# Kernel tuning notes

Measured on AMD Instinct MI355X. Metric: run time of the kernel, lower is better.

Reference implementation:

```python
import jax, jax.numpy as jnp
import numpy as np

B, N, D = 16, 512, 12
HID, HEADS = 32, 4
C = HID // HEADS  # per-head channels = 8


def setup_inputs() -> dict:
    key = jax.random.key(0)
    ks = jax.random.split(key, 12)
    s = 0.1
    return {
        "x": jax.random.normal(ks[0], (B, N, D), dtype=jnp.float32),
        "adj": jax.random.randint(ks[1], (B, N, N), 0, 2, dtype=jnp.int32),
        # node_proj: Linear(D, HID)
        "Wp": jax.random.normal(ks[2], (HID, D), dtype=jnp.float32) * s,
        "bp": jax.random.normal(ks[3], (HID,), dtype=jnp.float32) * s,
        # GATConv lin: Linear(HID, HEADS*C, bias=False)
        "Wg": jax.random.normal(ks[4], (HEADS * C, HID), dtype=jnp.float32) * s,
        "att_src": jax.random.normal(ks[5], (HEADS, C), dtype=jnp.float32) * s,
        "att_dst": jax.random.normal(ks[6], (HEADS, C), dtype=jnp.float32) * s,
        "bias_g": jax.random.normal(ks[7], (HEADS * C,), dtype=jnp.float32) * s,
        # edge_mlp: Linear(2*HID, HID) -> ReLU -> Linear(HID, 1) -> Sigmoid
        "W1": jax.random.normal(ks[8], (HID, 2 * HID), dtype=jnp.float32) * s,
        "b1": jax.random.normal(ks[9], (HID,), dtype=jnp.float32) * s,
        "w2": jax.random.normal(ks[10], (HID,), dtype=jnp.float32) * s,
        "b2": jax.random.normal(ks[11], (1,), dtype=jnp.float32) * s,
    }


def reference(x, adj, Wp, bp, Wg, att_src, att_dst, bias_g, W1, b1, w2, b2):
    Bq, Nq, _ = x.shape
    adj_b = adj != 0
    eye = jnp.eye(Nq, dtype=bool)

    # node_proj + ReLU
    h = jax.nn.relu(jnp.einsum('bnd,hd->bnh', x, Wp) + bp)  # [B,N,HID]

    # GATConv (PyG semantics): messages flow src=i (row) -> dst=j (col),
    # self-loops removed then re-added => diagonal forced on.
    g = jnp.einsum('bnd,kd->bnk', h, Wg).reshape(Bq, Nq, HEADS, C)  # [B,N,H,C]
    a_s = jnp.einsum('bnhc,hc->bnh', g, att_src)  # [B,N,H]
    a_d = jnp.einsum('bnhc,hc->bnh', g, att_dst)  # [B,N,H]
    logits = jax.nn.leaky_relu(a_s[:, :, None, :] + a_d[:, None, :, :], 0.2)  # [B,i,j,H]
    mask_sl = adj_b | eye
    logits = jnp.where(mask_sl[..., None], logits, -1e9)
    alpha = jax.nn.softmax(logits, axis=1)  # softmax over source i per target j
    h_gnn = jnp.einsum('bijh,bihc->bjhc', alpha, g).reshape(Bq, Nq, HEADS * C) + bias_g

    # edge MLP on all (i,j) pairs: cat([h_i, h_j]) -> split W1
    W1i, W1j = W1[:, :HID], W1[:, HID:]
    ti = jnp.einsum('bnd,hd->bnh', h_gnn, W1i)  # [B,N,HID] (row / i part)
    tj = jnp.einsum('bnd,hd->bnh', h_gnn, W1j)  # [B,N,HID] (col / j part)
    hidden = jax.nn.relu(ti[:, :, None, :] + tj[:, None, :, :] + b1)  # [B,N,N,HID]
    score = jax.nn.sigmoid(jnp.einsum('bijh,h->bij', hidden, w2) + b2[0])

    out_mask = adj_b & ~eye
    return jnp.where(out_mask, score, jnp.float32(0.0))
```

## Files before the change

kernel.cpp:

```cpp
#include <hip/hip_runtime.h>
#include <cstdint>

#define Bq 16
#define Nq 512
#define Dq 12
#define HID 32
#define HEADS 4
#define Cq 8

#define OFF_G     0u
#define OFF_AS    262144u
#define OFF_AD    294912u
#define OFF_TIT   327680u
#define OFF_TJB   589824u
#define OFF_PACK  851968u

__global__ __launch_bounds__(256) void k0_node(
    const float* __restrict__ x, const float* __restrict__ Wp, const float* __restrict__ bp,
    const float* __restrict__ Wg, const float* __restrict__ att_src,
    const float* __restrict__ att_dst, float* __restrict__ ws) {
    __shared__ float xs[8 * Dq];
    __shared__ float hs[8][HID];
    int n_sub = threadIdx.x >> 5;
    int k = threadIdx.x & 31;
    int node0 = blockIdx.x * 8;
    if (threadIdx.x < 8 * Dq) xs[threadIdx.x] = x[(size_t)node0 * Dq + threadIdx.x];
    __syncthreads();
    float s = bp[k];
#pragma unroll
    for (int d = 0; d < Dq; d++) s = fmaf(Wp[k * Dq + d], xs[n_sub * Dq + d], s);
    hs[n_sub][k] = s > 0.f ? s : 0.f;
    __syncthreads();
    float g = 0.f;
#pragma unroll
    for (int d = 0; d < HID; d++) g = fmaf(Wg[k * HID + d], hs[n_sub][d], g);
    int nid = node0 + n_sub;
    ws[OFF_G + (size_t)nid * HID + k] = g;
    float ss = g * att_src[k];
    float sd = g * att_dst[k];
#pragma unroll
    for (int off = 1; off < 8; off <<= 1) {
        ss += __shfl_xor(ss, off);
        sd += __shfl_xor(sd, off);
    }
    if ((k & 7) == 0) {
        int h = k >> 3;
        ws[OFF_AS + (size_t)nid * HEADS + h] = ss;
        ws[OFF_AD + (size_t)nid * HEADS + h] = sd;
    }
}

__global__ __launch_bounds__(256, 2) void k1_fused(
    const int* __restrict__ adj, const float* __restrict__ bias_g,
    const float* __restrict__ W1, const float* __restrict__ b1,
    float* __restrict__ ws) {
    int b = blockIdx.y;
    int j0 = blockIdx.x * 16;
    int t = threadIdx.x;
    int jl = t & 15;
    int ig = t >> 4;
    int j = j0 + jl;

    __shared__ float gs[64 * 36];
    __shared__ float ass[64 * 4];
    __shared__ float red[36 * 16 * 5];
    __shared__ float hgs[16 * 36];
    __shared__ float W1s[32 * 68];

    {
        const float4* src = (const float4*)W1;
        for (int k = t; k < 512; k += 256) {
            int h = k >> 4, q = k & 15;
            *(float4*)&W1s[h * 68 + q * 4] = src[k];
        }
    }
    float4 adv = *(const float4*)(ws + OFF_AD + ((size_t)b * Nq + j) * HEADS);

    float lsum[HEADS] = {0.f, 0.f, 0.f, 0.f};
    float acc[HEADS][Cq] = {};
    uint32_t mask = 0;

    const int* adjp = adj + ((size_t)b * Nq + ig) * Nq + j;
    const float* Gb = ws + OFF_G + (size_t)b * Nq * HID;
    const float* Ab = ws + OFF_AS + (size_t)b * Nq * HEADS;

    int cur[4], nxt[4];
#pragma unroll
    for (int kk = 0; kk < 4; kk++) cur[kk] = adjp[(size_t)(16 * kk) * Nq];

    for (int c = 0; c < 8; c++) {
        __syncthreads();
        {
            int ii = t >> 2, q = t & 3;
            const float4* s4 = (const float4*)(Gb + (size_t)(c * 64 + ii) * HID + q * 8);
            float4 v0 = s4[0], v1 = s4[1];
            *(float4*)&gs[ii * 36 + q * 8] = v0;
            *(float4*)&gs[ii * 36 + q * 8 + 4] = v1;
            if (t < 64)
                *(float4*)&ass[t * 4] = *(const float4*)(Ab + (size_t)(c * 64 + t) * HEADS);
        }
        if (c < 7) {
#pragma unroll
            for (int kk = 0; kk < 4; kk++)
                nxt[kk] = adjp[(size_t)(64 * (c + 1) + 16 * kk) * Nq];
        }
        __syncthreads();
#pragma unroll
        for (int kk = 0; kk < 4; kk++) {
            int m = 4 * c + kk;
            int i = 16 * m + ig;
            int a = cur[kk];
            bool msk = (a != 0) || (i == j);
            mask |= (uint32_t)(a != 0) << m;
            int ii = 16 * kk + ig;
            float4 asv = *(const float4*)&ass[ii * 4];
            const float* gr = &gs[ii * 36];
            float zs[HEADS] = {asv.x + adv.x, asv.y + adv.y, asv.z + adv.z, asv.w + adv.w};
#pragma unroll
            for (int h = 0; h < HEADS; h++) {
                float z = zs[h];
                float lk = z > 0.f ? z : 0.2f * z;
                float e = msk ? __expf(lk) : 0.f;
                lsum[h] += e;
                float4 g0 = *(const float4*)(gr + h * 8);
                float4 g1 = *(const float4*)(gr + h * 8 + 4);
                acc[h][0] = fmaf(e, g0.x, acc[h][0]);
                acc[h][1] = fmaf(e, g0.y, acc[h][1]);
                acc[h][2] = fmaf(e, g0.z, acc[h][2]);
                acc[h][3] = fmaf(e, g0.w, acc[h][3]);
                acc[h][4] = fmaf(e, g1.x, acc[h][4]);
                acc[h][5] = fmaf(e, g1.y, acc[h][5]);
                acc[h][6] = fmaf(e, g1.z, acc[h][6]);
                acc[h][7] = fmaf(e, g1.w, acc[h][7]);
            }
        }
#pragma unroll
        for (int kk = 0; kk < 4; kk++) cur[kk] = nxt[kk];
    }

    ((uint32_t*)(ws + OFF_PACK))[((size_t)b * Nq + j) * 16 + ig] = mask;

    int w = t >> 6;
    auto dump = [&](int r, float v) {
        v += __shfl_xor(v, 16);
        v += __shfl_xor(v, 32);
        if ((t & 63) < 16) red[(r * 16 + jl) * 5 + w] = v;
    };
#pragma unroll
    for (int h = 0; h < HEADS; h++) dump(h, lsum[h]);
#pragma unroll
    for (int h = 0; h < HEADS; h++)
#pragma unroll
        for (int cc = 0; cc < Cq; cc++) dump(4 + h * 8 + cc, acc[h][cc]);
    __syncthreads();
    for (int o = t; o < 576; o += 256) {
        float* p = &red[o * 5];
        p[4] = (p[0] + p[1]) + (p[2] + p[3]);
    }
    __syncthreads();
    for (int o = t; o < 512; o += 256) {
        int d = o >> 4, jj = o & 15;
        float s = red[((4 + d) * 16 + jj) * 5 + 4];
        float l = red[((d >> 3) * 16 + jj) * 5 + 4];
        hgs[jj * 36 + d] = s * __builtin_amdgcn_rcpf(l) + bias_g[d];
    }
    __syncthreads();
    {
        int tg = t >> 4;
        float si0 = 0.f, sj0 = 0.f, si1 = 0.f, sj1 = 0.f;
        const float* w0 = &W1s[tg * 68];
        const float* w1 = &W1s[(tg + 16) * 68];
        const float* hr = &hgs[jl * 36];
#pragma unroll
        for (int d = 0; d < HID; d++) {
            float hv = hr[d];
            si0 = fmaf(hv, w0[d], si0);
            sj0 = fmaf(hv, w0[32 + d], sj0);
            si1 = fmaf(hv, w1[d], si1);
            sj1 = fmaf(hv, w1[32 + d], sj1);
        }
        ws[OFF_TIT + ((size_t)b * HID + tg) * Nq + j] = si0;
        ws[OFF_TJB + ((size_t)b * HID + tg) * Nq + j] = sj0 + b1[tg];
        ws[OFF_TIT + ((size_t)b * HID + tg + 16) * Nq + j] = si1;
        ws[OFF_TJB + ((size_t)b * HID + tg + 16) * Nq + j] = sj1 + b1[tg + 16];
    }
}

__global__ __launch_bounds__(256) void k3_score(const float* __restrict__ w2_p,
                                                const float* __restrict__ b2_p,
                                                const float* __restrict__ ws,
                                                float* __restrict__ out) {
    int b = blockIdx.y;
    int i0 = blockIdx.x * 16;
    int j = threadIdx.x;
    __shared__ float tis[HID * 16];
    for (int t = threadIdx.x; t < HID * 16; t += 256) {
        int h = t >> 4, ii = t & 15;
        tis[t] = ws[OFF_TIT + ((size_t)b * HID + h) * Nq + i0 + ii];
    }
    float tjbA[HID], tjbB[HID];
#pragma unroll
    for (int h = 0; h < HID; h++) {
        const float* row = ws + OFF_TJB + ((size_t)b * HID + h) * Nq;
        tjbA[h] = row[j];
        tjbB[h] = row[j + 256];
    }
    float w2l[HID];
#pragma unroll
    for (int h = 0; h < HID; h++) w2l[h] = w2_p[h];
    float b2 = b2_p[0];
    const uint32_t* mrow = (const uint32_t*)(ws + OFF_PACK) + ((size_t)b * Nq + j) * 16;
    uint32_t mtA[16], mtB[16];
#pragma unroll
    for (int wq = 0; wq < 16; wq++) {
        mtA[wq] = mrow[wq];
        mtB[wq] = mrow[256 * 16 + wq];
    }
    int bit = i0 >> 4;
    __syncthreads();
    for (int ii = 0; ii < 16; ii++) {
        int i = i0 + ii;
        bool onA = (((mtA[ii] >> bit) & 1u) != 0) && (i != j);
        bool onB = (((mtB[ii] >> bit) & 1u) != 0) && (i != j + 256);
        float sA = b2, sB = b2;
#pragma unroll
        for (int h = 0; h < HID; h++) {
            float ti = tis[h * 16 + ii];
            float tA = ti + tjbA[h];
            tA = tA > 0.f ? tA : 0.f;
            sA = fmaf(tA, w2l[h], sA);
            float tB = ti + tjbB[h];
            tB = tB > 0.f ? tB : 0.f;
            sB = fmaf(tB, w2l[h], sB);
        }
        float scA = __builtin_amdgcn_rcpf(1.f + __expf(-sA));
        float scB = __builtin_amdgcn_rcpf(1.f + __expf(-sB));
        out[((size_t)b * Nq + i) * Nq + j] = onA ? scA : 0.f;
        out[((size_t)b * Nq + i) * Nq + j + 256] = onB ? scB : 0.f;
    }
}

extern "C" void kernel_launch(void* const* d_in, const int* in_sizes, int n_in,
                              void* d_out, int out_size, void* d_ws, size_t ws_size,
                              hipStream_t stream) {
    const float* x       = (const float*)d_in[0];
    const int*   adj     = (const int*)d_in[1];
    const float* Wp      = (const float*)d_in[2];
    const float* bp      = (const float*)d_in[3];
    const float* Wg      = (const float*)d_in[4];
    const float* att_src = (const float*)d_in[5];
    const float* att_dst = (const float*)d_in[6];
    const float* bias_g  = (const float*)d_in[7];
    const float* W1      = (const float*)d_in[8];
    const float* b1      = (const float*)d_in[9];
    const float* w2      = (const float*)d_in[10];
    const float* b2      = (const float*)d_in[11];
    float* out = (float*)d_out;
    float* ws = (float*)d_ws;
    (void)in_sizes; (void)n_in; (void)out_size; (void)ws_size;

    k0_node<<<dim3(1024), dim3(256), 0, stream>>>(x, Wp, bp, Wg, att_src, att_dst, ws);
    k1_fused<<<dim3(Nq / 16, Bq), dim3(256), 0, stream>>>(adj, bias_g, W1, b1, ws);
    k3_score<<<dim3(32, Bq), dim3(256), 0, stream>>>(w2, b2, ws, out);
}
```

Before: 133.3 us.

## Double-buffer G tiles in fused GAT kernel and transpose tj layout for score

The fused attention kernel now double-buffers the G and a_s tiles in one shared-memory arena. It prefetches the next chunk into registers during compute and drops one barrier per iteration. The tj+b1 table is staged through shared memory and written node-major so the score kernel can read it with float4 loads. The score kernel also uses a transposed ti tile with vector LDS reads, vectorized mask loads and a fully unrolled inner loop. The aim is to hide global-load latency and cut the score kernel's many scalar strided loads, at the cost of more register pressure and an extra sync plus staged write.

```diff
diff --git a/kernel.cpp b/kernel.cpp
--- a/kernel.cpp
+++ b/kernel.cpp
@@ -12,7 +12,7 @@
 #define OFF_AS    262144u
 #define OFF_AD    294912u
 #define OFF_TIT   327680u
-#define OFF_TJB   589824u
+#define OFF_TJBT  589824u
 #define OFF_PACK  851968u
 
 __global__ __launch_bounds__(256) void k0_node(
@@ -61,50 +61,51 @@
     int ig = t >> 4;
     int j = j0 + jl;
 
-    __shared__ float gs[64 * 36];
-    __shared__ float ass[64 * 4];
-    __shared__ float red[36 * 16 * 5];
-    __shared__ float hgs[16 * 36];
-    __shared__ float W1s[32 * 68];
-
+    __shared__ float smem[6176];
+    float* red = smem;
+    float* hgs = smem + 2880;
+    float* W1s = smem + 3456;
+    float* tjs = smem + 5632;
+
+    float4 adv = *(const float4*)(ws + OFF_AD + ((size_t)b * Nq + j) * HEADS);
+
+    const float* Gb = ws + OFF_G + (size_t)b * Nq * HID;
+    const float* Ab = ws + OFF_AS + (size_t)b * Nq * HEADS;
+    int ii_s = t >> 2, q_s = t & 3;
+
+    float4 ga, gb2;
+    float av;
     {
-        const float4* src = (const float4*)W1;
-        for (int k = t; k < 512; k += 256) {
-            int h = k >> 4, q = k & 15;
-            *(float4*)&W1s[h * 68 + q * 4] = src[k];
-        }
-    }
-    float4 adv = *(const float4*)(ws + OFF_AD + ((size_t)b * Nq + j) * HEADS);
+        const float* src = Gb + (size_t)ii_s * HID + q_s * 8;
+        ga = *(const float4*)src;
+        gb2 = *(const float4*)(src + 4);
+        av = Ab[t];
+        *(float4*)&smem[ii_s * 36 + q_s * 8] = ga;
+        *(float4*)&smem[ii_s * 36 + q_s * 8 + 4] = gb2;
+        smem[4608 + t] = av;
+    }
+    const int* adjp = adj + ((size_t)b * Nq + ig) * Nq + j;
+    int cur[4], nxt[4];
+#pragma unroll
+    for (int kk = 0; kk < 4; kk++) cur[kk] = adjp[(size_t)(16 * kk) * Nq];
 
     float lsum[HEADS] = {0.f, 0.f, 0.f, 0.f};
     float acc[HEADS][Cq] = {};
     uint32_t mask = 0;
 
-    const int* adjp = adj + ((size_t)b * Nq + ig) * Nq + j;
-    const float* Gb = ws + OFF_G + (size_t)b * Nq * HID;
-    const float* Ab = ws + OFF_AS + (size_t)b * Nq * HEADS;
-
-    int cur[4], nxt[4];
-#pragma unroll
-    for (int kk = 0; kk < 4; kk++) cur[kk] = adjp[(size_t)(16 * kk) * Nq];
-
     for (int c = 0; c < 8; c++) {
         __syncthreads();
-        {
-            int ii = t >> 2, q = t & 3;
-            const float4* s4 = (const float4*)(Gb + (size_t)(c * 64 + ii) * HID + q * 8);
-            float4 v0 = s4[0], v1 = s4[1];
-            *(float4*)&gs[ii * 36 + q * 8] = v0;
-            *(float4*)&gs[ii * 36 + q * 8 + 4] = v1;
-            if (t < 64)
-                *(float4*)&ass[t * 4] = *(const float4*)(Ab + (size_t)(c * 64 + t) * HEADS);
-        }
+        const float* gsc = (c & 1) ? smem + 2304 : smem;
+        const float* asc = (c & 1) ? smem + 4864 : smem + 4608;
         if (c < 7) {
+            const float* src = Gb + (size_t)((c + 1) * 64 + ii_s) * HID + q_s * 8;
+            ga = *(const float4*)src;
+            gb2 = *(const float4*)(src + 4);
+            av = Ab[(c + 1) * 256 + t];
 #pragma unroll
             for (int kk = 0; kk < 4; kk++)
                 nxt[kk] = adjp[(size_t)(64 * (c + 1) + 16 * kk) * Nq];
         }
-        __syncthreads();
 #pragma unroll
         for (int kk = 0; kk < 4; kk++) {
             int m = 4 * c + kk;
@@ -113,8 +114,8 @@
             bool msk = (a != 0) || (i == j);
             mask |= (uint32_t)(a != 0) << m;
             int ii = 16 * kk + ig;
-            float4 asv = *(const float4*)&ass[ii * 4];
-            const float* gr = &gs[ii * 36];
+            float4 asv = *(const float4*)&asc[ii * 4];
+            const float* gr = &gsc[ii * 36];
             float zs[HEADS] = {asv.x + adv.x, asv.y + adv.y, asv.z + adv.z, asv.w + adv.w};
 #pragma unroll
             for (int h = 0; h < HEADS; h++) {
@@ -134,12 +135,28 @@
                 acc[h][7] = fmaf(e, g1.w, acc[h][7]);
             }
         }
-#pragma unroll
-        for (int kk = 0; kk < 4; kk++) cur[kk] = nxt[kk];
+        if (c < 7) {
+            float* gsn = (c & 1) ? smem : smem + 2304;
+            float* asn = (c & 1) ? smem + 4608 : smem + 4864;
+            *(float4*)&gsn[ii_s * 36 + q_s * 8] = ga;
+            *(float4*)&gsn[ii_s * 36 + q_s * 8 + 4] = gb2;
+            asn[t] = av;
+#pragma unroll
+            for (int kk = 0; kk < 4; kk++) cur[kk] = nxt[kk];
+        }
     }
 
     ((uint32_t*)(ws + OFF_PACK))[((size_t)b * Nq + j) * 16 + ig] = mask;
 
+    __syncthreads();
+
+    {
+        const float4* src = (const float4*)W1;
+        for (int k = t; k < 512; k += 256) {
+            int h = k >> 4, q = k & 15;
+            *(float4*)&W1s[h * 68 + q * 4] = src[k];
+        }
+    }
     int w = t >> 6;
     auto dump = [&](int r, float v) {
         v += __shfl_xor(v, 16);
@@ -180,9 +197,14 @@
             sj1 = fmaf(hv, w1[32 + d], sj1);
         }
         ws[OFF_TIT + ((size_t)b * HID + tg) * Nq + j] = si0;
-        ws[OFF_TJB + ((size_t)b * HID + tg) * Nq + j] = sj0 + b1[tg];
         ws[OFF_TIT + ((size_t)b * HID + tg + 16) * Nq + j] = si1;
-        ws[OFF_TJB + ((size_t)b * HID + tg + 16) * Nq + j] = sj1 + b1[tg + 16];
+        tjs[tg * 17 + jl] = sj0 + b1[tg];
+        tjs[(tg + 16) * 17 + jl] = sj1 + b1[tg + 16];
+    }
+    __syncthreads();
+    for (int o = t; o < 512; o += 256) {
+        int jj = o >> 5, h = o & 31;
+        ws[OFF_TJBT + ((size_t)b * Nq + j0 + jj) * HID + h] = tjs[h * 17 + jj];
     }
 }
 
@@ -193,45 +215,58 @@
     int b = blockIdx.y;
     int i0 = blockIdx.x * 16;
     int j = threadIdx.x;
-    __shared__ float tis[HID * 16];
-    for (int t = threadIdx.x; t < HID * 16; t += 256) {
-        int h = t >> 4, ii = t & 15;
-        tis[t] = ws[OFF_TIT + ((size_t)b * HID + h) * Nq + i0 + ii];
-    }
-    float tjbA[HID], tjbB[HID];
-#pragma unroll
-    for (int h = 0; h < HID; h++) {
-        const float* row = ws + OFF_TJB + ((size_t)b * HID + h) * Nq;
-        tjbA[h] = row[j];
-        tjbB[h] = row[j + 256];
+    __shared__ float tisT[16 * 36];
+    {
+        int h = threadIdx.x >> 4, ii = threadIdx.x & 15;
+        tisT[ii * 36 + h] = ws[OFF_TIT + ((size_t)b * HID + h) * Nq + i0 + ii];
+        tisT[ii * 36 + h + 16] = ws[OFF_TIT + ((size_t)b * HID + h + 16) * Nq + i0 + ii];
+    }
+    float4 ta[8], tb[8];
+    const float* rA = ws + OFF_TJBT + ((size_t)b * Nq + j) * HID;
+    const float* rB = rA + (size_t)256 * HID;
+#pragma unroll
+    for (int q = 0; q < 8; q++) {
+        ta[q] = *(const float4*)(rA + q * 4);
+        tb[q] = *(const float4*)(rB + q * 4);
     }
     float w2l[HID];
 #pragma unroll
     for (int h = 0; h < HID; h++) w2l[h] = w2_p[h];
     float b2 = b2_p[0];
     const uint32_t* mrow = (const uint32_t*)(ws + OFF_PACK) + ((size_t)b * Nq + j) * 16;
-    uint32_t mtA[16], mtB[16];
-#pragma unroll
-    for (int wq = 0; wq < 16; wq++) {
-        mtA[wq] = mrow[wq];
-        mtB[wq] = mrow[256 * 16 + wq];
+    uint4 mAv[4], mBv[4];
+#pragma unroll
+    for (int q = 0; q < 4; q++) {
+        mAv[q] = ((const uint4*)mrow)[q];
+        mBv[q] = ((const uint4*)(mrow + 256 * 16))[q];
     }
     int bit = i0 >> 4;
     __syncthreads();
+#pragma unroll
     for (int ii = 0; ii < 16; ii++) {
         int i = i0 + ii;
-        bool onA = (((mtA[ii] >> bit) & 1u) != 0) && (i != j);
-        bool onB = (((mtB[ii] >> bit) & 1u) != 0) && (i != j + 256);
+        uint32_t mA = (ii & 3) == 0 ? mAv[ii >> 2].x : (ii & 3) == 1 ? mAv[ii >> 2].y
+                    : (ii & 3) == 2 ? mAv[ii >> 2].z : mAv[ii >> 2].w;
+        uint32_t mB = (ii & 3) == 0 ? mBv[ii >> 2].x : (ii & 3) == 1 ? mBv[ii >> 2].y
+                    : (ii & 3) == 2 ? mBv[ii >> 2].z : mBv[ii >> 2].w;
+        bool onA = (((mA >> bit) & 1u) != 0) && (i != j);
+        bool onB = (((mB >> bit) & 1u) != 0) && (i != j + 256);
         float sA = b2, sB = b2;
 #pragma unroll
-        for (int h = 0; h < HID; h++) {
-            float ti = tis[h * 16 + ii];
-            float tA = ti + tjbA[h];
-            tA = tA > 0.f ? tA : 0.f;
-            sA = fmaf(tA, w2l[h], sA);
-            float tB = ti + tjbB[h];
-            tB = tB > 0.f ? tB : 0.f;
-            sB = fmaf(tB, w2l[h], sB);
+        for (int q = 0; q < 8; q++) {
+            float4 tq = *(const float4*)&tisT[ii * 36 + q * 4];
+#pragma unroll
+            for (int e = 0; e < 4; e++) {
+                float ti = (e == 0) ? tq.x : (e == 1) ? tq.y : (e == 2) ? tq.z : tq.w;
+                float tjA = (e == 0) ? ta[q].x : (e == 1) ? ta[q].y : (e == 2) ? ta[q].z : ta[q].w;
+                float tjB = (e == 0) ? tb[q].x : (e == 1) ? tb[q].y : (e == 2) ? tb[q].z : tb[q].w;
+                float tA = ti + tjA;
+                tA = tA > 0.f ? tA : 0.f;
+                sA = fmaf(tA, w2l[q * 4 + e], sA);
+                float tB = ti + tjB;
+                tB = tB > 0.f ? tB : 0.f;
+                sB = fmaf(tB, w2l[q * 4 + e], sB);
+            }
         }
         float scA = __builtin_amdgcn_rcpf(1.f + __expf(-sA));
         float scB = __builtin_amdgcn_rcpf(1.f + __expf(-sB));
```

After: 128.5 us. 1.04x faster.
